# Optimization experiments

Measured on AMD Instinct MI355X. Metric: run time of the kernel, lower is better.

The kernel has to match this reference:

```python
import jax, jax.numpy as jnp
import numpy as np

# Module hyperparameters (init_kwargs)
H, W = 64, 64
STRIDE = 16
NUM_Y = (H - STRIDE) // STRIDE * 2 + 1   # 7
NUM_X = (W - STRIDE) // STRIDE * 2 + 1   # 7
NUM_POS = NUM_Y * NUM_X - 1              # 48 (use_origin=False)
CHAN_PER_POS = 8
C = NUM_POS * CHAN_PER_POS               # 384
B = 32
K = 3        # LO_kernel_size
SIGMA = 0.5  # LO_sigma


def _init_offset():
    # Mirrors DisplaceChannel.init_offset for fill=False, use_origin=False,
    # actual_stride=None, random_offset=0.
    offs = []
    for ih in range(-(NUM_Y // 2), NUM_Y // 2 + 1):
        for iw in range(-(NUM_X // 2), NUM_X // 2 + 1):
            if ih == 0 and iw == 0:
                continue
            offs.append([iw * STRIDE, ih * STRIDE])  # (x, y)
    return np.asarray(offs, dtype=np.float32)      # [NUM_POS, 2]


def setup_inputs() -> dict:
    key = jax.random.key(0)
    k1, k2 = jax.random.split(key)
    inp = jax.random.normal(k1, (B, C, H, W), dtype=jnp.float32)
    # Learned offsets: grid init plus sub-pixel perturbation (exercises the
    # learnable-offset Gaussian kernel with nonzero fractional part).
    offset = jnp.asarray(_init_offset()) + jax.random.uniform(
        k2, (NUM_POS, 2), minval=-0.45, maxval=0.45, dtype=jnp.float32)
    return {"inp": inp, "offset": offset}


def _displace(x, off_int):
    # x: [B, C, H, W]; off_int: [P, 2] int32 (x, y) per channel group.
    # out[b, p, cp, y, x] = x[b, p, cp, y - oy, x - ox], zero outside (fill=False).
    xg = x.reshape(B, NUM_POS, CHAN_PER_POS, H, W)
    ox, oy = off_int[:, 0], off_int[:, 1]                # [P]
    ys = jnp.arange(H)[None, :] - oy[:, None]            # [P, H]
    xs = jnp.arange(W)[None, :] - ox[:, None]            # [P, W]
    vy = (ys >= 0) & (ys < H)
    vx = (xs >= 0) & (xs < W)
    ysc = jnp.clip(ys, 0, H - 1)
    xsc = jnp.clip(xs, 0, W - 1)
    g = jnp.take_along_axis(xg, ysc[None, :, None, :, None], axis=3)
    g = jnp.take_along_axis(g, xsc[None, :, None, None, :], axis=4)
    mask = (vy[:, :, None] & vx[:, None, :])[None, :, None, :, :]
    return jnp.where(mask, g, 0.0).reshape(B, C, H, W)


def reference(inp, offset):
    # Integer displacement uses detached rounded offsets.
    off_round = jax.lax.stop_gradient(jnp.round(offset))
    out = _displace(inp, off_round.astype(jnp.int32))

    # Learnable-offset path: per-position Gaussian kernel centered at the
    # fractional offset remainder, applied as a depthwise conv.
    frac = offset - off_round                                   # [P, 2]
    coords = jnp.arange(K, dtype=jnp.float32) - float(K // 2)   # [K]
    field_x = jnp.broadcast_to(coords[None, :], (K, K))         # x varies along axis 1
    field_y = jnp.broadcast_to(coords[:, None], (K, K))
    dx = field_x[None] + frac[:, None, None, 0]                 # [P, K, K]
    dy = field_y[None] + frac[:, None, None, 1]
    kern = jnp.exp(-(dx * dx + dy * dy) / (2.0 * SIGMA ** 2))
    kern = kern / jnp.sum(kern, axis=(1, 2), keepdims=True)
    kern = jnp.repeat(kern[:, None, :, :], CHAN_PER_POS, axis=1)
    kern = kern.reshape(C, 1, K, K)                             # depthwise OIHW
    out = jax.lax.conv_general_dilated(
        out, kern, window_strides=(1, 1),
        padding=[(K // 2, K // 2), (K // 2, K // 2)],
        dimension_numbers=("NCHW", "OIHW", "NCHW"),
        feature_group_count=C)
    return out
```

## Files before the change

kernel.cpp:

```cpp
#include <hip/hip_runtime.h>


constexpr int HH = 64;
constexpr int WW = 64;
constexpr int B_ = 32;
constexpr int C_ = 384;
constexpr int PLANES = B_ * C_;
constexpr long long NELEM = (long long)PLANES * HH * WW;

__global__ __launch_bounds__(256) void displace_conv_v2(
    const float* __restrict__ inp, const float* __restrict__ offset,
    float* __restrict__ out) {
  const int plane = blockIdx.x;
  const int c = plane % C_;
  const int pos = c >> 3;

  const float offx = offset[2 * pos + 0];
  const float offy = offset[2 * pos + 1];
  const float rx = rintf(offx);
  const float ry = rintf(offy);
  const int ox = (int)rx;
  const int oy = (int)ry;
  const float fx = offx - rx;
  const float fy = offy - ry;

  float gx0 = __expf(-2.f * (fx - 1.f) * (fx - 1.f));
  float gx1 = __expf(-2.f * fx * fx);
  float gx2 = __expf(-2.f * (fx + 1.f) * (fx + 1.f));
  const float sxi = 1.f / (gx0 + gx1 + gx2);
  gx0 *= sxi; gx1 *= sxi; gx2 *= sxi;

  float gy0 = __expf(-2.f * (fy - 1.f) * (fy - 1.f));
  float gy1 = __expf(-2.f * fy * fy);
  float gy2 = __expf(-2.f * (fy + 1.f) * (fy + 1.f));
  const float syi = 1.f / (gy0 + gy1 + gy2);
  gy0 *= syi; gy1 *= syi; gy2 *= syi;

  const int t = threadIdx.x;
  const int cg = t & 15;
  const int rg = t >> 4;
  const int x4 = cg << 2;
  const int y0 = rg << 2;

  const int xlo = ox > 0 ? ox : 0;
  const int xhi = ox < 0 ? WW + ox : WW;
  const int ylo = oy > 0 ? oy : 0;
  const int yhi = oy < 0 ? HH + oy : HH;

  const int q = x4 - 1 - ox;
  float vm[6];
#pragma unroll
  for (int m = 0; m < 6; ++m) {
    const int xt = x4 - 1 + m;
    vm[m] = (xt >= xlo && xt < xhi) ? 1.f : 0.f;
  }

  const float* __restrict__ pbase = inp + (size_t)plane * (HH * WW);
  float* __restrict__ obase = out + (size_t)plane * (HH * WW);
  const float* const lo = inp;
  const float* const hi = inp + (NELEM - 8);

  auto hrow = [&](int ty) -> float4 {
    const float rs = (ty >= ylo && ty < yhi) ? 1.f : 0.f;
    int tsrc = ty - oy;
    tsrc = tsrc < 0 ? 0 : (tsrc > HH - 1 ? HH - 1 : tsrc);
    const float* p = pbase + tsrc * WW + q;
    p = p < lo ? lo : (p > hi ? hi : p);
    float s[8];
    __builtin_memcpy(&s[0], p, 16);
    __builtin_memcpy(&s[4], p + 4, 16);
#pragma unroll
    for (int m = 0; m < 6; ++m) s[m] *= vm[m];
    float4 r;
    r.x = rs * (gx0 * s[0] + gx1 * s[1] + gx2 * s[2]);
    r.y = rs * (gx0 * s[1] + gx1 * s[2] + gx2 * s[3]);
    r.z = rs * (gx0 * s[2] + gx1 * s[3] + gx2 * s[4]);
    r.w = rs * (gx0 * s[3] + gx1 * s[4] + gx2 * s[5]);
    return r;
  };

  float4 a = hrow(y0 - 1);
  float4 b = hrow(y0);
#pragma unroll
  for (int i = 0; i < 4; ++i) {
    const float4 cc = hrow(y0 + 1 + i);
    float4 o;
    o.x = gy0 * a.x + gy1 * b.x + gy2 * cc.x;
    o.y = gy0 * a.y + gy1 * b.y + gy2 * cc.y;
    o.z = gy0 * a.z + gy1 * b.z + gy2 * cc.z;
    o.w = gy0 * a.w + gy1 * b.w + gy2 * cc.w;
    *(float4*)(obase + (y0 + i) * WW + x4) = o;
    a = b;
    b = cc;
  }
}

extern "C" void kernel_launch(void* const* d_in, const int* in_sizes, int n_in,
                              void* d_out, int out_size, void* d_ws, size_t ws_size,
                              hipStream_t stream) {
  const float* inp = (const float*)d_in[0];
  const float* offset = (const float*)d_in[1];
  float* out = (float*)d_out;
  displace_conv_v2<<<PLANES, 256, 0, stream>>>(inp, offset, out);
}
```

Baseline: 319.6 us.

## Stage displaced input plane in LDS with zero halo before stencil

Each block now loads its whole displaced 64x64 input plane once into shared memory, with masking applied at load time and a zero-padded halo, then computes the separable 3x3 Gaussian from LDS. This removes the redundant overlapping global loads (each row read by several threads for neighbouring output rows and the halo) and the per-load masking. It adds a block-wide barrier and about 20 KB of LDS per block, which may reduce occupancy.

```diff
diff --git a/kernel.cpp b/kernel.cpp
--- a/kernel.cpp
+++ b/kernel.cpp
@@ -7,10 +7,14 @@
 constexpr int C_ = 384;
 constexpr int PLANES = B_ * C_;
 constexpr long long NELEM = (long long)PLANES * HH * WW;
+constexpr int LSTR = 76;
+constexpr int GL = 3;
 
-__global__ __launch_bounds__(256) void displace_conv_v2(
+__global__ __launch_bounds__(256) void displace_conv_v3(
     const float* __restrict__ inp, const float* __restrict__ offset,
     float* __restrict__ out) {
+  __shared__ float lds[66 * LSTR];
+
   const int plane = blockIdx.x;
   const int c = plane % C_;
   const int pos = c >> 3;
@@ -37,45 +41,57 @@
   gy0 *= syi; gy1 *= syi; gy2 *= syi;
 
   const int t = threadIdx.x;
-  const int cg = t & 15;
-  const int rg = t >> 4;
-  const int x4 = cg << 2;
-  const int y0 = rg << 2;
 
-  const int xlo = ox > 0 ? ox : 0;
-  const int xhi = ox < 0 ? WW + ox : WW;
-  const int ylo = oy > 0 ? oy : 0;
-  const int yhi = oy < 0 ? HH + oy : HH;
-
-  const int q = x4 - 1 - ox;
-  float vm[6];
-#pragma unroll
-  for (int m = 0; m < 6; ++m) {
-    const int xt = x4 - 1 + m;
-    vm[m] = (xt >= xlo && xt < xhi) ? 1.f : 0.f;
+  if (t < LSTR) {
+    lds[t] = 0.f;
+    lds[65 * LSTR + t] = 0.f;
+  }
+  if (t < 64) {
+    lds[(t + 1) * LSTR + 3] = 0.f;
+    lds[(t + 1) * LSTR + 68] = 0.f;
   }
 
-  const float* __restrict__ pbase = inp + (size_t)plane * (HH * WW);
+  {
+    const int r = t >> 2;
+    const int d0 = (t & 3) << 4;
+    const bool rowok = (unsigned)(r - oy) < (unsigned)HH;
+    int rc = r - oy;
+    rc = rc < 0 ? 0 : (rc > HH - 1 ? HH - 1 : rc);
+    const float* p = inp + (size_t)plane * (HH * WW) + rc * WW + (d0 - ox);
+    const float* const lo = inp;
+    const float* const hi = inp + (NELEM - 16);
+    p = p < lo ? lo : (p > hi ? hi : p);
+    float s[16];
+    __builtin_memcpy(&s[0], p, 16);
+    __builtin_memcpy(&s[4], p + 4, 16);
+    __builtin_memcpy(&s[8], p + 8, 16);
+    __builtin_memcpy(&s[12], p + 12, 16);
+    float v[16];
+#pragma unroll
+    for (int j = 0; j < 16; ++j) {
+      const bool ok = rowok && ((unsigned)(d0 + j - ox) < (unsigned)WW);
+      v[j] = ok ? s[j] : 0.f;
+    }
+    float* dst = &lds[(r + 1) * LSTR + 4 + d0];
+#pragma unroll
+    for (int j = 0; j < 4; ++j)
+      *(float4*)(dst + 4 * j) =
+          make_float4(v[4 * j], v[4 * j + 1], v[4 * j + 2], v[4 * j + 3]);
+  }
+
+  __syncthreads();
+
+  const int x4 = (t & 15) << 2;
+  const int y0 = (t >> 4) << 2;
   float* __restrict__ obase = out + (size_t)plane * (HH * WW);
-  const float* const lo = inp;
-  const float* const hi = inp + (NELEM - 8);
 
   auto hrow = [&](int ty) -> float4 {
-    const float rs = (ty >= ylo && ty < yhi) ? 1.f : 0.f;
-    int tsrc = ty - oy;
-    tsrc = tsrc < 0 ? 0 : (tsrc > HH - 1 ? HH - 1 : tsrc);
-    const float* p = pbase + tsrc * WW + q;
-    p = p < lo ? lo : (p > hi ? hi : p);
-    float s[8];
-    __builtin_memcpy(&s[0], p, 16);
-    __builtin_memcpy(&s[4], p + 4, 16);
-#pragma unroll
-    for (int m = 0; m < 6; ++m) s[m] *= vm[m];
+    const float* p = &lds[(ty + 1) * LSTR + GL + x4];
     float4 r;
-    r.x = rs * (gx0 * s[0] + gx1 * s[1] + gx2 * s[2]);
-    r.y = rs * (gx0 * s[1] + gx1 * s[2] + gx2 * s[3]);
-    r.z = rs * (gx0 * s[2] + gx1 * s[3] + gx2 * s[4]);
-    r.w = rs * (gx0 * s[3] + gx1 * s[4] + gx2 * s[5]);
+    r.x = gx0 * p[0] + gx1 * p[1] + gx2 * p[2];
+    r.y = gx0 * p[1] + gx1 * p[2] + gx2 * p[3];
+    r.z = gx0 * p[2] + gx1 * p[3] + gx2 * p[4];
+    r.w = gx0 * p[3] + gx1 * p[4] + gx2 * p[5];
     return r;
   };
 
@@ -101,5 +117,5 @@
   const float* inp = (const float*)d_in[0];
   const float* offset = (const float*)d_in[1];
   float* out = (float*)d_out;
-  displace_conv_v2<<<PLANES, 256, 0, stream>>>(inp, offset, out);
+  displace_conv_v3<<<PLANES, 256, 0, stream>>>(inp, offset, out);
 }
```

After: 327.8 us. 1.03x slower.
